# Kernel optimization log

Measured on AMD Instinct MI355X. Metric: run time of the kernel, lower is better.

Reference implementation:

```python
import jax, jax.numpy as jnp
import numpy as np

N_HEAD = 16
MASK_VALUE = -10000.0


def setup_inputs() -> dict:
    key = jax.random.key(0)
    k1, k2, k3 = jax.random.split(key, 3)
    B, S, D = 2, 2048, 1024
    x = jax.random.normal(k1, (B, S, D), dtype=jnp.float32)
    W_qkv = jax.random.normal(k2, (D, 3 * D), dtype=jnp.float32) * 0.02
    b_qkv = jnp.zeros((3 * D,), dtype=jnp.float32)
    W_out = jax.random.normal(k3, (D, D), dtype=jnp.float32) * 0.02
    b_out = jnp.zeros((D,), dtype=jnp.float32)
    return {"x": x, "W_qkv": W_qkv, "b_qkv": b_qkv, "W_out": W_out, "b_out": b_out}


def reference(x, W_qkv, b_qkv, W_out, b_out):
    B, S, D = x.shape
    H = N_HEAD
    hd = D // H
    # fused QKV projection
    qkv = x @ W_qkv + b_qkv                      # [B, S, 3D]
    q, k, v = jnp.split(qkv, 3, axis=-1)
    # split heads -> [B, H, S, hd]
    def split_heads(t):
        return t.reshape(B, S, H, hd).transpose(0, 2, 1, 3)
    q, k, v = split_heads(q), split_heads(k), split_heads(v)
    # scaled causal attention with explicit mask-fill (matches ops.attention)
    scale = 1.0 / jnp.sqrt(jnp.asarray(hd, dtype=x.dtype))
    w = jnp.einsum('bhqd,bhkd->bhqk', q, k) * scale   # [B, H, S, S]
    causal = jnp.tril(jnp.ones((S, S), dtype=bool))    # [S, S]
    w = jnp.where(causal, w, jnp.asarray(MASK_VALUE, dtype=w.dtype))
    a = jax.nn.softmax(w, axis=-1)
    o = jnp.einsum('bhqk,bhkd->bhqd', a, v)            # [B, H, S, hd]
    # merge heads -> [B, S, D]
    o = o.transpose(0, 2, 1, 3).reshape(B, S, D)
    out = o @ W_out + b_out
    return out
```

## Files before the change

### kernel.cpp

```cpp
#include <hip/hip_runtime.h>
#include <hip/hip_bf16.h>
#include <stdint.h>

#define BATCH 2
#define SEQ   2048
#define DIM   1024
#define NH    16
#define HD    64
#define MVAL  (-10000.0f)

#if __has_builtin(__builtin_amdgcn_exp2f)
#define EXP2(x) __builtin_amdgcn_exp2f(x)
#define QSCALE  (0.125f * 1.44269504f)
#else
#define EXP2(x) __expf(x)
#define QSCALE  0.125f
#endif

typedef __attribute__((ext_vector_type(8))) short bf16x8;
typedef __attribute__((ext_vector_type(4))) float f32x4;
typedef unsigned short u16;

static __device__ __forceinline__ u16 f2bf(float f) {
  union { float f; uint32_t u; } c; c.f = f;
  uint32_t x = c.u;
  return (u16)((x + 0x7fffu + ((x >> 16) & 1u)) >> 16);
}

static __device__ __forceinline__ uint32_t pk2(float a, float b) {
  __hip_bfloat162 h = __float22bfloat162_rn(make_float2(a, b));
  union { __hip_bfloat162 h; uint32_t u; } c; c.h = h;
  return c.u;
}

static __device__ __forceinline__ int swz128(int row, int chunk) {
  return row * 128 + (((chunk ^ (row & 7)) & 7) << 4);
}

static __device__ __forceinline__ void gload_lds16(const void* g, void* l) {
  __builtin_amdgcn_global_load_lds((const __attribute__((address_space(1))) void*)g,
                                   (__attribute__((address_space(3))) void*)l, 16, 0, 0);
}

__global__ void prep_kernel(const float* __restrict__ x, u16* __restrict__ xb,
                            const float* __restrict__ Wqkv, u16* __restrict__ WqkvT,
                            const float* __restrict__ Wout, u16* __restrict__ WoutT) {
  __shared__ float tile[32][33];
  int blk = blockIdx.x, tid = threadIdx.x;
  if (blk < 4096) {
    int i = blk * 256 + tid;
    float4 v = reinterpret_cast<const float4*>(x)[i];
    reinterpret_cast<uint2*>(xb)[i] = make_uint2(pk2(v.x, v.y), pk2(v.z, v.w));
    return;
  }
  const float* in;
  u16* out;
  int C, t;
  if (blk < 4096 + 3072) { t = blk - 4096; in = Wqkv; out = WqkvT; C = 3072; }
  else                   { t = blk - 7168; in = Wout; out = WoutT; C = 1024; }
  int R = DIM;
  int c0 = (t % (C / 32)) * 32, r0 = (t / (C / 32)) * 32;
  int tx = tid & 31, ty = tid >> 5;
#pragma unroll
  for (int i = 0; i < 32; i += 8)
    tile[ty + i][tx] = in[(size_t)(r0 + ty + i) * C + c0 + tx];
  __syncthreads();
#pragma unroll
  for (int i = 0; i < 32; i += 8)
    out[(size_t)(c0 + ty + i) * R + r0 + tx] = f2bf(tile[tx][ty + i]);
}

__global__ void vtrans_kernel(const u16* __restrict__ Vi, u16* __restrict__ Vo) {
  __shared__ __align__(16) char t[8192];
  int tid = threadIdx.x;
  int bh = blockIdx.y, s0 = blockIdx.x * 64;
  const u16* src = Vi + ((size_t)bh * SEQ + s0) * HD;
#pragma unroll
  for (int i = 0; i < 2; i++) {
    int r = i * 32 + (tid >> 3), ch = tid & 7;
    uint4 v = *reinterpret_cast<const uint4*>(src + (size_t)r * HD + ch * 8);
    *reinterpret_cast<uint4*>(t + swz128(r, ch)) = v;
  }
  __syncthreads();
  int d = tid >> 2, sc = tid & 3;
  u16 vals[16];
#pragma unroll
  for (int j = 0; j < 16; j++) {
    int s = sc * 16 + j;
    vals[j] = *reinterpret_cast<const u16*>(
        t + s * 128 + ((((d >> 3) ^ (s & 7)) & 7) << 4) + (d & 7) * 2);
  }
  u16* dst = Vo + ((size_t)bh * HD + d) * SEQ + s0 + sc * 16;
  *reinterpret_cast<uint4*>(dst) = *reinterpret_cast<const uint4*>(vals);
  *reinterpret_cast<uint4*>(dst + 8) = *reinterpret_cast<const uint4*>(vals + 8);
}

template <int EPI>
__global__ __launch_bounds__(256, 2) void gemm_bt_kernel(
    const u16* __restrict__ A, const u16* __restrict__ Bt,
    const float* __restrict__ bias, float* __restrict__ Cout,
    u16* __restrict__ Qo, u16* __restrict__ Ko, u16* __restrict__ Vo,
    int M, int N, int K) {
  __shared__ __align__(16) char lds[32768];
  char* As = lds;
  char* Bs = lds + 16384;
  int tid = threadIdx.x;
  int lane = tid & 63, l15 = lane & 15, l4 = lane >> 4;
  int w = tid >> 6, wr = w >> 1, wc = w & 1;
  int m0 = blockIdx.y * 128, n0 = blockIdx.x * 128;
  int srow = tid >> 3, sch = tid & 7;
  int sc_swz = ((sch ^ (srow & 7)) << 3);

  const u16* Ap = A + (size_t)(m0 + srow) * K + sc_swz;
  const u16* Bp = Bt + (size_t)(n0 + srow) * K + sc_swz;

  f32x4 acc[4][4] = {};

  for (int k0 = 0; k0 < K; k0 += 64) {
    __syncthreads();
#pragma unroll
    for (int i = 0; i < 4; i++) {
      gload_lds16(Ap + (size_t)i * 32 * K + k0, As + i * 4096 + tid * 16);
      gload_lds16(Bp + (size_t)i * 32 * K + k0, Bs + i * 4096 + tid * 16);
    }
    __syncthreads();
#pragma unroll
    for (int ks = 0; ks < 2; ks++) {
      int ch = ks * 4 + l4;
      bf16x8 af[4], bfv[4];
#pragma unroll
      for (int mi = 0; mi < 4; mi++)
        af[mi] = *reinterpret_cast<const bf16x8*>(As + swz128(wr * 64 + mi * 16 + l15, ch));
#pragma unroll
      for (int nj = 0; nj < 4; nj++)
        bfv[nj] = *reinterpret_cast<const bf16x8*>(Bs + swz128(wc * 64 + nj * 16 + l15, ch));
#pragma unroll
      for (int nj = 0; nj < 4; nj++)
#pragma unroll
        for (int mi = 0; mi < 4; mi++)
          acc[nj][mi] = __builtin_amdgcn_mfma_f32_16x16x32_bf16(bfv[nj], af[mi], acc[nj][mi], 0, 0, 0);
    }
  }

#pragma unroll
  for (int nj = 0; nj < 4; nj++) {
    int nb = n0 + wc * 64 + nj * 16 + l4 * 4;
    float4 bv = *reinterpret_cast<const float4*>(bias + nb);
#pragma unroll
    for (int mi = 0; mi < 4; mi++) {
      int m = m0 + wr * 64 + mi * 16 + l15;
      f32x4 a = acc[nj][mi];
      float v0 = a[0] + bv.x, v1 = a[1] + bv.y, v2 = a[2] + bv.z, v3 = a[3] + bv.w;
      if (EPI == 1) {
        *reinterpret_cast<float4*>(Cout + (size_t)m * N + nb) = make_float4(v0, v1, v2, v3);
      } else {
        int b = m >> 11, s = m & 2047;
        int sec = nb >> 10, c = nb & 1023, h = c >> 6, d = c & 63;
        size_t bh = (size_t)(b * NH + h);
        u16* dst;
        float scl;
        if (sec == 0)      { dst = Qo; scl = QSCALE; }
        else if (sec == 1) { dst = Ko; scl = 1.0f; }
        else               { dst = Vo; scl = 1.0f; }
        *reinterpret_cast<uint2*>(dst + (bh * SEQ + s) * HD + d) =
            make_uint2(pk2(v0 * scl, v1 * scl), pk2(v2 * scl, v3 * scl));
      }
    }
  }
}

__global__ __launch_bounds__(256, 2) void attn_kernel(
    const u16* __restrict__ Q, const u16* __restrict__ K,
    const u16* __restrict__ Vt, u16* __restrict__ O) {
  __shared__ __align__(16) char lds[81920];
  int tid = threadIdx.x, lane = tid & 63, w = tid >> 6;
  int l15 = lane & 15, l4 = lane >> 4;
  int sub = w & 1, par = w >> 1;
  int blk = blockIdx.x;
  int bh = (blk & 7) * 4 + ((blk >> 3) & 3);
  int p = blk >> 5;
  const u16* Qh = Q + (size_t)bh * SEQ * HD;
  const u16* Kh = K + (size_t)bh * SEQ * HD;
  const u16* Vh = Vt + (size_t)bh * HD * SEQ;
  char* Pw = lds + 65536 + w * 4096;
  int srow = tid >> 3, sch = tid & 7;
  int b_ = bh >> 4, h_ = bh & 15;

  bf16x8 onesf;
#pragma unroll
  for (int j = 0; j < 8; j++) onesf[j] = (short)0x3F80;

  auto stageKV = [&](int b, int T) {
    const u16* Kt = Kh + (size_t)T * 128 * HD;
    const u16* Vs = Vh + (size_t)T * 128;
    char* Kb = lds + b * 16384;
    char* Vb = lds + 32768 + b * 16384;
#pragma unroll
    for (int i = 0; i < 4; i++) {
      int row = i * 32 + srow;
      int c = (sch ^ (row & 7)) << 3;
      gload_lds16(Kt + (size_t)row * HD + c, Kb + row * 128 + sch * 16);
    }
#pragma unroll
    for (int sv = 0; sv < 2; sv++)
#pragma unroll
      for (int i = 0; i < 2; i++) {
        int d = i * 32 + srow;
        int c = (sch ^ (d & 7)) << 3;
        gload_lds16(Vs + (size_t)d * SEQ + sv * 64 + c, Vb + sv * 8192 + d * 128 + sch * 16);
      }
  };

  int buf = 0;
  stageKV(0, 0);
  __syncthreads();

  for (int pass = 0; pass < 2; pass++) {
    int qt = (pass == 0) ? (31 - p) : p;
    int nT = (qt + 2) >> 1;
    int qb = qt * 64 + sub * 32;

    bf16x8 qf[2][2];
#pragma unroll
    for (int mi = 0; mi < 2; mi++)
#pragma unroll
      for (int ks = 0; ks < 2; ks++)
        qf[mi][ks] = *reinterpret_cast<const bf16x8*>(
            Qh + (size_t)(qb + mi * 16 + l15) * HD + ks * 32 + l4 * 8);

    float mrun[2] = {-1e30f, -1e30f};
    f32x4 oacc[4][2] = {};
    f32x4 acc_l[2] = {};
    bf16x8 pf_c[2][2], vf_c[4][2];
    bool pend = false;

    for (int T = 0; T < nT; T++) {
      int nxt = (T + 1 < nT) ? (T + 1) : (pass == 0 ? 0 : -1);
      if (nxt >= 0) stageKV(buf ^ 1, nxt);

      char* Kw = lds + buf * 16384 + par * 8192;
      char* Vw = lds + 32768 + buf * 16384 + par * 8192;
      int kvb = T * 128 + par * 64;

      __builtin_amdgcn_s_setprio(1);
      if (pend) {
#pragma unroll
        for (int ks = 0; ks < 2; ks++) {
#pragma unroll
          for (int nd = 0; nd < 4; nd++)
#pragma unroll
            for (int mi = 0; mi < 2; mi++)
              oacc[nd][mi] = __builtin_amdgcn_mfma_f32_16x16x32_bf16(
                  vf_c[nd][ks], pf_c[mi][ks], oacc[nd][mi], 0, 0, 0);
#pragma unroll
          for (int mi = 0; mi < 2; mi++)
            acc_l[mi] = __builtin_amdgcn_mfma_f32_16x16x32_bf16(
                onesf, pf_c[mi][ks], acc_l[mi], 0, 0, 0);
        }
      }

      f32x4 s[4][2] = {};
#pragma unroll
      for (int ks = 0; ks < 2; ks++)
#pragma unroll
        for (int nj = 0; nj < 4; nj++) {
          bf16x8 kf = *reinterpret_cast<const bf16x8*>(Kw + swz128(nj * 16 + l15, ks * 4 + l4));
#pragma unroll
          for (int mi = 0; mi < 2; mi++)
            s[nj][mi] = __builtin_amdgcn_mfma_f32_16x16x32_bf16(kf, qf[mi][ks], s[nj][mi], 0, 0, 0);
        }
      __builtin_amdgcn_s_setprio(0);

#pragma unroll
      for (int ks = 0; ks < 2; ks++)
#pragma unroll
        for (int nd = 0; nd < 4; nd++)
          vf_c[nd][ks] = *reinterpret_cast<const bf16x8*>(Vw + swz128(nd * 16 + l15, ks * 4 + l4));

      if (kvb + 63 > qb) {
#pragma unroll
        for (int nj = 0; nj < 4; nj++)
#pragma unroll
          for (int mi = 0; mi < 2; mi++) {
            int qg = qb + mi * 16 + l15;
#pragma unroll
            for (int r = 0; r < 4; r++) {
              int kg = kvb + nj * 16 + l4 * 4 + r;
              if (kg > qg) s[nj][mi][r] = MVAL;
            }
          }
      }

      float mt[2];
#pragma unroll
      for (int mi = 0; mi < 2; mi++) {
        float m = s[0][mi][0];
#pragma unroll
        for (int nj = 0; nj < 4; nj++)
#pragma unroll
          for (int r = 0; r < 4; r++) m = fmaxf(m, s[nj][mi][r]);
        m = fmaxf(m, __shfl_xor(m, 16));
        m = fmaxf(m, __shfl_xor(m, 32));
        mt[mi] = m;
      }

      if (!__all((mt[0] <= mrun[0]) & (mt[1] <= mrun[1]))) {
#pragma unroll
        for (int mi = 0; mi < 2; mi++) {
          float mnew = fmaxf(mrun[mi], mt[mi]);
          float alpha = EXP2(mrun[mi] - mnew);
          mrun[mi] = mnew;
#pragma unroll
          for (int nd = 0; nd < 4; nd++)
#pragma unroll
            for (int r = 0; r < 4; r++) oacc[nd][mi][r] *= alpha;
#pragma unroll
          for (int r = 0; r < 4; r++) acc_l[mi][r] *= alpha;
        }
      }

#pragma unroll
      for (int mi = 0; mi < 2; mi++) {
        int prow = mi * 16 + l15;
#pragma unroll
        for (int nj = 0; nj < 4; nj++) {
          float p0 = EXP2(s[nj][mi][0] - mrun[mi]);
          float p1 = EXP2(s[nj][mi][1] - mrun[mi]);
          float p2 = EXP2(s[nj][mi][2] - mrun[mi]);
          float p3 = EXP2(s[nj][mi][3] - mrun[mi]);
          int chunk = nj * 2 + (l4 >> 1);
          char* dst = Pw + prow * 128 + (((chunk ^ (prow & 7)) & 7) << 4) + (l4 & 1) * 8;
          *reinterpret_cast<uint2*>(dst) = make_uint2(pk2(p0, p1), pk2(p2, p3));
        }
      }

      asm volatile("s_waitcnt lgkmcnt(0)" ::: "memory");
      __builtin_amdgcn_sched_barrier(0);

#pragma unroll
      for (int mi = 0; mi < 2; mi++)
#pragma unroll
        for (int ks = 0; ks < 2; ks++)
          pf_c[mi][ks] = *reinterpret_cast<const bf16x8*>(Pw + swz128(mi * 16 + l15, ks * 4 + l4));
      pend = true;

      __syncthreads();
      buf ^= 1;
    }

    __builtin_amdgcn_s_setprio(1);
#pragma unroll
    for (int ks = 0; ks < 2; ks++) {
#pragma unroll
      for (int nd = 0; nd < 4; nd++)
#pragma unroll
        for (int mi = 0; mi < 2; mi++)
          oacc[nd][mi] = __builtin_amdgcn_mfma_f32_16x16x32_bf16(
              vf_c[nd][ks], pf_c[mi][ks], oacc[nd][mi], 0, 0, 0);
#pragma unroll
      for (int mi = 0; mi < 2; mi++)
        acc_l[mi] = __builtin_amdgcn_mfma_f32_16x16x32_bf16(
            onesf, pf_c[mi][ks], acc_l[mi], 0, 0, 0);
    }
    __builtin_amdgcn_s_setprio(0);

    char* Xo = lds + (buf ^ 1) * 16384;
    float* Xml = (float*)(lds + 65536);
    if (par == 1) {
#pragma unroll
      for (int mi = 0; mi < 2; mi++) {
        int row = sub * 32 + mi * 16 + l15;
        if (l4 == 0) {
          Xml[row * 2] = mrun[mi];
          Xml[row * 2 + 1] = acc_l[mi][0];
        }
#pragma unroll
        for (int nd = 0; nd < 4; nd++)
          *reinterpret_cast<f32x4*>(Xo + row * 256 + (((nd * 4 + l4) ^ (row & 7)) << 4)) =
              oacc[nd][mi];
      }
    }
    __syncthreads();
    if (par == 0) {
#pragma unroll
      for (int mi = 0; mi < 2; mi++) {
        int row = sub * 32 + mi * 16 + l15;
        float mB = Xml[row * 2], lB = Xml[row * 2 + 1];
        float m = fmaxf(mrun[mi], mB);
        float wA = EXP2(mrun[mi] - m), wB = EXP2(mB - m);
        float linv = 1.0f / (acc_l[mi][0] * wA + lB * wB);
        float fA = wA * linv, fB = wB * linv;
        u16* orow = O + ((size_t)b_ * SEQ + qt * 64 + sub * 32 + mi * 16 + l15) * DIM + h_ * HD;
#pragma unroll
        for (int nd = 0; nd < 4; nd++) {
          f32x4 ob = *reinterpret_cast<const f32x4*>(
              Xo + row * 256 + (((nd * 4 + l4) ^ (row & 7)) << 4));
          float o0 = oacc[nd][mi][0] * fA + ob[0] * fB;
          float o1 = oacc[nd][mi][1] * fA + ob[1] * fB;
          float o2 = oacc[nd][mi][2] * fA + ob[2] * fB;
          float o3 = oacc[nd][mi][3] * fA + ob[3] * fB;
          *reinterpret_cast<uint2*>(orow + nd * 16 + l4 * 4) = make_uint2(pk2(o0, o1), pk2(o2, o3));
        }
      }
    }
    __syncthreads();
  }
}

extern "C" void kernel_launch(void* const* d_in, const int* in_sizes, int n_in,
                              void* d_out, int out_size, void* d_ws, size_t ws_size,
                              hipStream_t stream) {
  const float* x     = (const float*)d_in[0];
  const float* W_qkv = (const float*)d_in[1];
  const float* b_qkv = (const float*)d_in[2];
  const float* W_out = (const float*)d_in[3];
  const float* b_out = (const float*)d_in[4];
  float* out = (float*)d_out;
  char* ws = (char*)d_ws;

  u16* xb    = (u16*)(ws);
  u16* WqkvT = (u16*)(ws + 8388608);
  u16* WoutT = (u16*)(ws + 8388608 + 6291456);
  u16* Qb    = (u16*)(ws + 16777216);
  u16* Kb    = (u16*)(ws + 16777216 + 8388608);
  u16* Vtb   = (u16*)(ws + 16777216 + 2 * 8388608);
  u16* Ob    = (u16*)(ws + 16777216 + 3 * 8388608);
  u16* Vraw  = Ob;

  prep_kernel<<<4096 + 3072 + 1024, 256, 0, stream>>>(x, xb, W_qkv, WqkvT, W_out, WoutT);
  gemm_bt_kernel<0><<<dim3(3 * DIM / 128, BATCH * SEQ / 128), 256, 0, stream>>>(
      xb, WqkvT, b_qkv, nullptr, Qb, Kb, Vraw, BATCH * SEQ, 3 * DIM, DIM);
  vtrans_kernel<<<dim3(SEQ / 64, BATCH * NH), 256, 0, stream>>>(Vraw, Vtb);
  attn_kernel<<<512, 256, 0, stream>>>(Qb, Kb, Vtb, Ob);
  gemm_bt_kernel<1><<<dim3(DIM / 128, BATCH * SEQ / 128), 256, 0, stream>>>(
      Ob, WoutT, b_out, out, nullptr, nullptr, nullptr, BATCH * SEQ, DIM, DIM);
}
```

Measured before the change: 116.9 us.

## Switch attention to 32x32x16 MFMA with register-resident P via permlane swap

Rewrites the attention inner loop to use 32x32x16 bf16 MFMA tiles instead of 16x16x32, so each wave handles one 32-row query tile with a single running max and sum. The P matrix is repacked in registers with v_permlane32_swap instead of a round trip through LDS, which shrinks LDS from 80KB to 64KB. The row sum is now computed on the vector ALU instead of an extra MFMA against a ones vector. The gains meant here are fewer LDS writes and reads, less MFMA issue overhead and no waitcnt stall. The costs are more scalar exp/add work per lane and reliance on a gfx950-specific permlane instruction with a correct lane mapping.

```diff
diff --git a/kernel.cpp b/kernel.cpp
--- a/kernel.cpp
+++ b/kernel.cpp
@@ -19,6 +19,7 @@
 
 typedef __attribute__((ext_vector_type(8))) short bf16x8;
 typedef __attribute__((ext_vector_type(4))) float f32x4;
+typedef __attribute__((ext_vector_type(16))) float f32x16;
 typedef unsigned short u16;
 
 static __device__ __forceinline__ u16 f2bf(float f) {
@@ -172,9 +173,9 @@
 __global__ __launch_bounds__(256, 2) void attn_kernel(
     const u16* __restrict__ Q, const u16* __restrict__ K,
     const u16* __restrict__ Vt, u16* __restrict__ O) {
-  __shared__ __align__(16) char lds[81920];
+  __shared__ __align__(16) char lds[65536];
   int tid = threadIdx.x, lane = tid & 63, w = tid >> 6;
-  int l15 = lane & 15, l4 = lane >> 4;
+  int l31 = lane & 31, hi = lane >> 5;
   int sub = w & 1, par = w >> 1;
   int blk = blockIdx.x;
   int bh = (blk & 7) * 4 + ((blk >> 3) & 3);
@@ -182,13 +183,8 @@
   const u16* Qh = Q + (size_t)bh * SEQ * HD;
   const u16* Kh = K + (size_t)bh * SEQ * HD;
   const u16* Vh = Vt + (size_t)bh * HD * SEQ;
-  char* Pw = lds + 65536 + w * 4096;
   int srow = tid >> 3, sch = tid & 7;
   int b_ = bh >> 4, h_ = bh & 15;
-
-  bf16x8 onesf;
-#pragma unroll
-  for (int j = 0; j < 8; j++) onesf[j] = (short)0x3F80;
 
   auto stageKV = [&](int b, int T) {
     const u16* Kt = Kh + (size_t)T * 128 * HD;
@@ -220,18 +216,15 @@
     int nT = (qt + 2) >> 1;
     int qb = qt * 64 + sub * 32;
 
-    bf16x8 qf[2][2];
-#pragma unroll
-    for (int mi = 0; mi < 2; mi++)
-#pragma unroll
-      for (int ks = 0; ks < 2; ks++)
-        qf[mi][ks] = *reinterpret_cast<const bf16x8*>(
-            Qh + (size_t)(qb + mi * 16 + l15) * HD + ks * 32 + l4 * 8);
-
-    float mrun[2] = {-1e30f, -1e30f};
-    f32x4 oacc[4][2] = {};
-    f32x4 acc_l[2] = {};
-    bf16x8 pf_c[2][2], vf_c[4][2];
+    bf16x8 qf[4];
+#pragma unroll
+    for (int ks = 0; ks < 4; ks++)
+      qf[ks] = *reinterpret_cast<const bf16x8*>(
+          Qh + (size_t)(qb + l31) * HD + ks * 16 + hi * 8);
+
+    float mrun = -1e30f, lrun = 0.0f;
+    f32x16 oacc[2] = {};
+    bf16x8 pf_c[4], vf_c[2][4];
     bool pend = false;
 
     for (int T = 0; T < nT; T++) {
@@ -245,103 +238,87 @@
       __builtin_amdgcn_s_setprio(1);
       if (pend) {
 #pragma unroll
-        for (int ks = 0; ks < 2; ks++) {
-#pragma unroll
-          for (int nd = 0; nd < 4; nd++)
-#pragma unroll
-            for (int mi = 0; mi < 2; mi++)
-              oacc[nd][mi] = __builtin_amdgcn_mfma_f32_16x16x32_bf16(
-                  vf_c[nd][ks], pf_c[mi][ks], oacc[nd][mi], 0, 0, 0);
-#pragma unroll
-          for (int mi = 0; mi < 2; mi++)
-            acc_l[mi] = __builtin_amdgcn_mfma_f32_16x16x32_bf16(
-                onesf, pf_c[mi][ks], acc_l[mi], 0, 0, 0);
-        }
-      }
-
-      f32x4 s[4][2] = {};
-#pragma unroll
-      for (int ks = 0; ks < 2; ks++)
-#pragma unroll
-        for (int nj = 0; nj < 4; nj++) {
-          bf16x8 kf = *reinterpret_cast<const bf16x8*>(Kw + swz128(nj * 16 + l15, ks * 4 + l4));
-#pragma unroll
-          for (int mi = 0; mi < 2; mi++)
-            s[nj][mi] = __builtin_amdgcn_mfma_f32_16x16x32_bf16(kf, qf[mi][ks], s[nj][mi], 0, 0, 0);
+        for (int ks = 0; ks < 4; ks++)
+#pragma unroll
+          for (int nd = 0; nd < 2; nd++)
+            oacc[nd] = __builtin_amdgcn_mfma_f32_32x32x16_bf16(
+                vf_c[nd][ks], pf_c[ks], oacc[nd], 0, 0, 0);
+      }
+
+      f32x16 s[2] = {};
+#pragma unroll
+      for (int ks = 0; ks < 4; ks++)
+#pragma unroll
+        for (int n = 0; n < 2; n++) {
+          bf16x8 kf = *reinterpret_cast<const bf16x8*>(
+              Kw + swz128(n * 32 + l31, 2 * ks + hi));
+          s[n] = __builtin_amdgcn_mfma_f32_32x32x16_bf16(kf, qf[ks], s[n], 0, 0, 0);
         }
       __builtin_amdgcn_s_setprio(0);
 
 #pragma unroll
-      for (int ks = 0; ks < 2; ks++)
-#pragma unroll
-        for (int nd = 0; nd < 4; nd++)
-          vf_c[nd][ks] = *reinterpret_cast<const bf16x8*>(Vw + swz128(nd * 16 + l15, ks * 4 + l4));
+      for (int nd = 0; nd < 2; nd++)
+#pragma unroll
+        for (int ks = 0; ks < 4; ks++)
+          vf_c[nd][ks] = *reinterpret_cast<const bf16x8*>(
+              Vw + swz128(nd * 32 + l31, 2 * ks + hi));
 
       if (kvb + 63 > qb) {
-#pragma unroll
-        for (int nj = 0; nj < 4; nj++)
-#pragma unroll
-          for (int mi = 0; mi < 2; mi++) {
-            int qg = qb + mi * 16 + l15;
-#pragma unroll
-            for (int r = 0; r < 4; r++) {
-              int kg = kvb + nj * 16 + l4 * 4 + r;
-              if (kg > qg) s[nj][mi][r] = MVAL;
-            }
+        int qg = qb + l31;
+#pragma unroll
+        for (int n = 0; n < 2; n++)
+#pragma unroll
+          for (int r = 0; r < 16; r++) {
+            int kg = kvb + n * 32 + (r & 3) + 8 * (r >> 2) + 4 * hi;
+            if (kg > qg) s[n][r] = MVAL;
           }
       }
 
-      float mt[2];
-#pragma unroll
-      for (int mi = 0; mi < 2; mi++) {
-        float m = s[0][mi][0];
-#pragma unroll
-        for (int nj = 0; nj < 4; nj++)
-#pragma unroll
-          for (int r = 0; r < 4; r++) m = fmaxf(m, s[nj][mi][r]);
-        m = fmaxf(m, __shfl_xor(m, 16));
-        m = fmaxf(m, __shfl_xor(m, 32));
-        mt[mi] = m;
-      }
-
-      if (!__all((mt[0] <= mrun[0]) & (mt[1] <= mrun[1]))) {
-#pragma unroll
-        for (int mi = 0; mi < 2; mi++) {
-          float mnew = fmaxf(mrun[mi], mt[mi]);
-          float alpha = EXP2(mrun[mi] - mnew);
-          mrun[mi] = mnew;
-#pragma unroll
-          for (int nd = 0; nd < 4; nd++)
-#pragma unroll
-            for (int r = 0; r < 4; r++) oacc[nd][mi][r] *= alpha;
-#pragma unroll
-          for (int r = 0; r < 4; r++) acc_l[mi][r] *= alpha;
+      float mt = s[0][0];
+#pragma unroll
+      for (int n = 0; n < 2; n++)
+#pragma unroll
+        for (int r = 0; r < 16; r++) mt = fmaxf(mt, s[n][r]);
+      mt = fmaxf(mt, __shfl_xor(mt, 32));
+
+      if (!__all(mt <= mrun)) {
+        float mnew = fmaxf(mrun, mt);
+        float alpha = EXP2(mrun - mnew);
+        mrun = mnew;
+#pragma unroll
+        for (int nd = 0; nd < 2; nd++)
+#pragma unroll
+          for (int r = 0; r < 16; r++) oacc[nd][r] *= alpha;
+        lrun *= alpha;
+      }
+
+      float rs = 0.0f;
+#pragma unroll
+      for (int n = 0; n < 2; n++)
+#pragma unroll
+        for (int r = 0; r < 16; r++) {
+          float pv = EXP2(s[n][r] - mrun);
+          s[n][r] = pv;
+          rs += pv;
         }
-      }
-
-#pragma unroll
-      for (int mi = 0; mi < 2; mi++) {
-        int prow = mi * 16 + l15;
-#pragma unroll
-        for (int nj = 0; nj < 4; nj++) {
-          float p0 = EXP2(s[nj][mi][0] - mrun[mi]);
-          float p1 = EXP2(s[nj][mi][1] - mrun[mi]);
-          float p2 = EXP2(s[nj][mi][2] - mrun[mi]);
-          float p3 = EXP2(s[nj][mi][3] - mrun[mi]);
-          int chunk = nj * 2 + (l4 >> 1);
-          char* dst = Pw + prow * 128 + (((chunk ^ (prow & 7)) & 7) << 4) + (l4 & 1) * 8;
-          *reinterpret_cast<uint2*>(dst) = make_uint2(pk2(p0, p1), pk2(p2, p3));
+      rs += __shfl_xor(rs, 32);
+      lrun += rs;
+
+#pragma unroll
+      for (int n = 0; n < 2; n++)
+#pragma unroll
+        for (int half = 0; half < 2; half++) {
+          int rb = half * 8;
+          uint32_t a0 = pk2(s[n][rb + 0], s[n][rb + 1]);
+          uint32_t b0 = pk2(s[n][rb + 4], s[n][rb + 5]);
+          asm("v_permlane32_swap_b32 %0, %1" : "+v"(a0), "+v"(b0));
+          uint32_t a1 = pk2(s[n][rb + 2], s[n][rb + 3]);
+          uint32_t b1 = pk2(s[n][rb + 6], s[n][rb + 7]);
+          asm("v_permlane32_swap_b32 %0, %1" : "+v"(a1), "+v"(b1));
+          union { uint32_t u[4]; bf16x8 v; } bw;
+          bw.u[0] = a0; bw.u[1] = a1; bw.u[2] = b0; bw.u[3] = b1;
+          pf_c[n * 2 + half] = bw.v;
         }
-      }
-
-      asm volatile("s_waitcnt lgkmcnt(0)" ::: "memory");
-      __builtin_amdgcn_sched_barrier(0);
-
-#pragma unroll
-      for (int mi = 0; mi < 2; mi++)
-#pragma unroll
-        for (int ks = 0; ks < 2; ks++)
-          pf_c[mi][ks] = *reinterpret_cast<const bf16x8*>(Pw + swz128(mi * 16 + l15, ks * 4 + l4));
       pend = true;
 
       __syncthreads();
@@ -350,58 +327,54 @@
 
     __builtin_amdgcn_s_setprio(1);
 #pragma unroll
-    for (int ks = 0; ks < 2; ks++) {
-#pragma unroll
-      for (int nd = 0; nd < 4; nd++)
-#pragma unroll
-        for (int mi = 0; mi < 2; mi++)
-          oacc[nd][mi] = __builtin_amdgcn_mfma_f32_16x16x32_bf16(
-              vf_c[nd][ks], pf_c[mi][ks], oacc[nd][mi], 0, 0, 0);
-#pragma unroll
-      for (int mi = 0; mi < 2; mi++)
-        acc_l[mi] = __builtin_amdgcn_mfma_f32_16x16x32_bf16(
-            onesf, pf_c[mi][ks], acc_l[mi], 0, 0, 0);
-    }
+    for (int ks = 0; ks < 4; ks++)
+#pragma unroll
+      for (int nd = 0; nd < 2; nd++)
+        oacc[nd] = __builtin_amdgcn_mfma_f32_32x32x16_bf16(
+            vf_c[nd][ks], pf_c[ks], oacc[nd], 0, 0, 0);
     __builtin_amdgcn_s_setprio(0);
 
     char* Xo = lds + (buf ^ 1) * 16384;
-    float* Xml = (float*)(lds + 65536);
+    float* Xml = (float*)(lds + 32768 + (buf ^ 1) * 16384);
+    int row = sub * 32 + l31;
     if (par == 1) {
-#pragma unroll
-      for (int mi = 0; mi < 2; mi++) {
-        int row = sub * 32 + mi * 16 + l15;
-        if (l4 == 0) {
-          Xml[row * 2] = mrun[mi];
-          Xml[row * 2 + 1] = acc_l[mi][0];
+      if (hi == 0) {
+        Xml[row * 2] = mrun;
+        Xml[row * 2 + 1] = lrun;
+      }
+#pragma unroll
+      for (int nd = 0; nd < 2; nd++)
+#pragma unroll
+        for (int g = 0; g < 4; g++) {
+          int chunk = 8 * nd + 2 * g + hi;
+          f32x4 t;
+          t[0] = oacc[nd][4 * g];     t[1] = oacc[nd][4 * g + 1];
+          t[2] = oacc[nd][4 * g + 2]; t[3] = oacc[nd][4 * g + 3];
+          *reinterpret_cast<f32x4*>(Xo + row * 256 + (((chunk ^ (row & 7)) & 15) << 4)) = t;
         }
-#pragma unroll
-        for (int nd = 0; nd < 4; nd++)
-          *reinterpret_cast<f32x4*>(Xo + row * 256 + (((nd * 4 + l4) ^ (row & 7)) << 4)) =
-              oacc[nd][mi];
-      }
     }
     __syncthreads();
     if (par == 0) {
-#pragma unroll
-      for (int mi = 0; mi < 2; mi++) {
-        int row = sub * 32 + mi * 16 + l15;
-        float mB = Xml[row * 2], lB = Xml[row * 2 + 1];
-        float m = fmaxf(mrun[mi], mB);
-        float wA = EXP2(mrun[mi] - m), wB = EXP2(mB - m);
-        float linv = 1.0f / (acc_l[mi][0] * wA + lB * wB);
-        float fA = wA * linv, fB = wB * linv;
-        u16* orow = O + ((size_t)b_ * SEQ + qt * 64 + sub * 32 + mi * 16 + l15) * DIM + h_ * HD;
-#pragma unroll
-        for (int nd = 0; nd < 4; nd++) {
+      float mB = Xml[row * 2], lB = Xml[row * 2 + 1];
+      float m = fmaxf(mrun, mB);
+      float wA = EXP2(mrun - m), wB = EXP2(mB - m);
+      float linv = 1.0f / (lrun * wA + lB * wB);
+      float fA = wA * linv, fB = wB * linv;
+      u16* orow = O + ((size_t)b_ * SEQ + qb + l31) * DIM + h_ * HD;
+#pragma unroll
+      for (int nd = 0; nd < 2; nd++)
+#pragma unroll
+        for (int g = 0; g < 4; g++) {
+          int chunk = 8 * nd + 2 * g + hi;
           f32x4 ob = *reinterpret_cast<const f32x4*>(
-              Xo + row * 256 + (((nd * 4 + l4) ^ (row & 7)) << 4));
-          float o0 = oacc[nd][mi][0] * fA + ob[0] * fB;
-          float o1 = oacc[nd][mi][1] * fA + ob[1] * fB;
-          float o2 = oacc[nd][mi][2] * fA + ob[2] * fB;
-          float o3 = oacc[nd][mi][3] * fA + ob[3] * fB;
-          *reinterpret_cast<uint2*>(orow + nd * 16 + l4 * 4) = make_uint2(pk2(o0, o1), pk2(o2, o3));
+              Xo + row * 256 + (((chunk ^ (row & 7)) & 15) << 4));
+          float o0 = oacc[nd][4 * g] * fA + ob[0] * fB;
+          float o1 = oacc[nd][4 * g + 1] * fA + ob[1] * fB;
+          float o2 = oacc[nd][4 * g + 2] * fA + ob[2] * fB;
+          float o3 = oacc[nd][4 * g + 3] * fA + ob[3] * fB;
+          int d0 = nd * 32 + 8 * g + 4 * hi;
+          *reinterpret_cast<uint2*>(orow + d0) = make_uint2(pk2(o0, o1), pk2(o2, o3));
         }
-      }
     }
     __syncthreads();
   }
```

Result: no change. 116.2 us (-0.6%).
